# Performance work log

Hardware: AMD Instinct MI355X
Metric: run time of the kernel (lower is better)

The kernel has to match this reference:

```python
import jax, jax.numpy as jnp
import numpy as np

B, S, D, H = 4, 2048, 1024, 16
HD = D // H  # head_dim = 64


def setup_inputs() -> dict:
    key = jax.random.key(0)
    ks = jax.random.split(key, 5)
    scale = 0.02
    return {
        "x": jax.random.normal(ks[0], (B, S, D), dtype=jnp.float32),
        "Wq": jax.random.normal(ks[1], (D, D), dtype=jnp.float32) * scale,
        "Wk": jax.random.normal(ks[2], (D, D), dtype=jnp.float32) * scale,
        "Wv": jax.random.normal(ks[3], (D, D), dtype=jnp.float32) * scale,
        "Wo": jax.random.normal(ks[4], (D, D), dtype=jnp.float32) * scale,
        "bo": jnp.zeros((D,), dtype=jnp.float32),
    }


def reference(x, Wq, Wk, Wv, Wo, bo):
    b, s, d = x.shape
    # projections (no bias on q/k/v, matching qkv_bias=False)
    q = (x @ Wq).reshape(b, s, H, HD).transpose(0, 2, 1, 3)  # [B,H,S,HD]
    k = (x @ Wk).reshape(b, s, H, HD).transpose(0, 2, 1, 3)
    v = (x @ Wv).reshape(b, s, H, HD).transpose(0, 2, 1, 3)
    scores = jnp.einsum("bhqd,bhkd->bhqk", q, k) / jnp.sqrt(jnp.float32(HD))
    causal = jnp.tril(jnp.ones((s, s), dtype=bool))  # True = keep
    scores = jnp.where(causal, scores, -jnp.inf)
    attn = jax.nn.softmax(scores, axis=-1)
    # dropout p=0.0 -> identity
    out = jnp.einsum("bhqk,bhkd->bhqd", attn, v)
    out = out.transpose(0, 2, 1, 3).reshape(b, s, d)
    return out @ Wo + bo
```

## Files before the change

kernel.cpp:

```cpp
#include <hip/hip_runtime.h>

typedef unsigned short u16;
typedef unsigned int u32;
typedef __attribute__((ext_vector_type(4))) float f32x4;
typedef __attribute__((ext_vector_type(8))) __bf16 bf16x8;
typedef __attribute__((ext_vector_type(4))) _Float16 f16x4;
typedef __attribute__((ext_vector_type(4))) u16 u16x4;
typedef __attribute__((ext_vector_type(4))) u32 u32x4;
typedef __attribute__((ext_vector_type(2))) u32 u32x2;

#define D_ 1024
#define S_ 2048
#define B_ 4
#define H_ 16
#define HD_ 64
#define M_ 8192
#define LDP 72
#define QSCALE 0.18033688011112042591f

__device__ __forceinline__ u16 f2bf(float f) {
  u32 u = __float_as_uint(f);
  u += 0x7fffu + ((u >> 16) & 1u);
  return (u16)(u >> 16);
}

__device__ __forceinline__ float max3f(float a, float b, float c) {
  return fmaxf(fmaxf(a, b), c);
}

__device__ __forceinline__ void gload_lds16(const void* g, void* l) {
  __builtin_amdgcn_global_load_lds((const __attribute__((address_space(1))) void*)g,
                                   (__attribute__((address_space(3))) void*)l, 16, 0, 0);
}

__global__ __launch_bounds__(256) void cast_x_kernel(const float* __restrict__ x,
                                                     u16* __restrict__ xb) {
  int i = (blockIdx.x * 256 + threadIdx.x) * 4;
  f32x4 v = *(const f32x4*)(x + i);
  u16x4 o = {f2bf(v[0]), f2bf(v[1]), f2bf(v[2]), f2bf(v[3])};
  *(u16x4*)(xb + i) = o;
}

__global__ __launch_bounds__(256) void wtrans_kernel(const float* __restrict__ Wq, const float* __restrict__ Wk,
                                                     const float* __restrict__ Wv, const float* __restrict__ Wo,
                                                     u16* __restrict__ Wqt, u16* __restrict__ Wkt,
                                                     u16* __restrict__ Wvt, u16* __restrict__ Wot) {
  __shared__ float lds[64][65];
  const float* W = blockIdx.z == 0 ? Wq : blockIdx.z == 1 ? Wk : blockIdx.z == 2 ? Wv : Wo;
  u16* Wt       = blockIdx.z == 0 ? Wqt : blockIdx.z == 1 ? Wkt : blockIdx.z == 2 ? Wvt : Wot;
  int k0 = blockIdx.x * 64, n0 = blockIdx.y * 64;
  int tr = threadIdx.x >> 6, tc = threadIdx.x & 63;
#pragma unroll
  for (int i = 0; i < 16; ++i)
    lds[tr + i * 4][tc] = W[(size_t)(k0 + tr + i * 4) * D_ + n0 + tc];
  __syncthreads();
#pragma unroll
  for (int i = 0; i < 16; ++i)
    Wt[(size_t)(n0 + tr + i * 4) * D_ + k0 + tc] = f2bf(lds[tc][tr + i * 4]);
}

__device__ __forceinline__ void gemm_main(const u16* __restrict__ A, const u16* __restrict__ Bt,
                                          u16* As, u16* Bs, int row0, int col0, f32x4 acc[4][4]) {
  const int tid = threadIdx.x;
  const int lane = tid & 63, wave = tid >> 6;
  const int wr = wave >> 1, wc = wave & 1;
  const int l15 = lane & 15, lg = lane >> 4;
  const int sr8 = lane >> 3;
  const int scx = (lane & 7) ^ sr8;
#pragma unroll 1
  for (int k0 = 0; k0 < D_; k0 += 64) {
#pragma unroll
    for (int it = 0; it < 4; ++it) {
      int rbase = (it * 4 + wave) * 8;
      int r = rbase + sr8;
      gload_lds16(A + (size_t)(row0 + r) * D_ + k0 + scx * 8, As + rbase * 64);
      gload_lds16(Bt + (size_t)(col0 + r) * D_ + k0 + scx * 8, Bs + rbase * 64);
    }
    __syncthreads();
#pragma unroll
    for (int kk = 0; kk < 64; kk += 32) {
      const int cb = kk >> 3;
      bf16x8 af[4], bf[4];
#pragma unroll
      for (int m = 0; m < 4; ++m) {
        int row = wr * 64 + m * 16 + l15;
        af[m] = *(const bf16x8*)(As + row * 64 + (((cb + lg) ^ (l15 & 7)) << 3));
      }
#pragma unroll
      for (int n = 0; n < 4; ++n) {
        int row = wc * 64 + n * 16 + l15;
        bf[n] = *(const bf16x8*)(Bs + row * 64 + (((cb + lg) ^ (l15 & 7)) << 3));
      }
#pragma unroll
      for (int m = 0; m < 4; ++m)
#pragma unroll
        for (int n = 0; n < 4; ++n)
          acc[m][n] = __builtin_amdgcn_mfma_f32_16x16x32_bf16(af[m], bf[n], acc[m][n], 0, 0, 0);
    }
    __syncthreads();
  }
}

__global__ __launch_bounds__(256) void qkv_gemm_kernel(const u16* __restrict__ xb,
                                                       const u16* __restrict__ Wqt, const u16* __restrict__ Wkt,
                                                       const u16* __restrict__ Wvt,
                                                       u16* __restrict__ Qb, u16* __restrict__ Kb,
                                                       _Float16* __restrict__ Vt) {
  __shared__ u16 As[128 * 64];
  __shared__ u16 Bs[128 * 64];
  int lin = blockIdx.x;
  int xcd = lin & 7, pos = lin >> 3;
  int mode = pos / 64;
  int rem = pos & 63;
  int by = xcd * 8 + (rem >> 3);
  int bx = rem & 7;
  const u16* Bt = mode == 0 ? Wqt : mode == 1 ? Wkt : Wvt;
  f32x4 acc[4][4] = {};
  int row0 = by * 128, col0 = bx * 128;
  gemm_main(xb, Bt, As, Bs, row0, col0, acc);
  int lane = threadIdx.x & 63, wave = threadIdx.x >> 6;
  int wr = wave >> 1, wc = wave & 1, l15 = lane & 15, lg = lane >> 4;
  int rbase = row0 + wr * 64 + lg * 4, cbase = col0 + wc * 64 + l15;
  if (mode == 2) {
#pragma unroll
    for (int m = 0; m < 4; ++m) {
      int row = rbase + m * 16;
      int b = row >> 11, s = row & (S_ - 1);
#pragma unroll
      for (int n = 0; n < 4; ++n) {
        int col = cbase + n * 16;
        int h = col >> 6, hd = col & 63;
        f16x4 vv = {(_Float16)acc[m][n][0], (_Float16)acc[m][n][1],
                    (_Float16)acc[m][n][2], (_Float16)acc[m][n][3]};
        *(f16x4*)(Vt + ((size_t)((b << 4) + h) * HD_ + hd) * S_ + s) = vv;
      }
    }
  } else {
    u16* dst = mode == 0 ? Qb : Kb;
    float scl = mode == 0 ? QSCALE : 1.0f;
#pragma unroll
    for (int m = 0; m < 4; ++m)
#pragma unroll
      for (int n = 0; n < 4; ++n) {
        int col = cbase + n * 16;
#pragma unroll
        for (int r = 0; r < 4; ++r) {
          int row = rbase + m * 16 + r;
          dst[(size_t)row * D_ + col] = f2bf(acc[m][n][r] * scl);
        }
      }
  }
}

__global__ __launch_bounds__(256) void attn_kernel(const u16* __restrict__ Qb, const u16* __restrict__ Kb,
                                                   const _Float16* __restrict__ Vt, u16* __restrict__ attnb) {
  __shared__ u16 Ks[2][64][LDP];
  __shared__ _Float16 Vs[2][HD_][LDP];
  const int tid = threadIdx.x;
  const int wave = tid >> 6, lane = tid & 63;
  const int l15 = lane & 15, lg = lane >> 4;
  const int lin = blockIdx.x;
  const int xcd = lin & 7, slot = lin >> 3;
  const int p = slot >> 3;
  const int bh = (slot & 7) * 8 + xcd;
  const int b = bh >> 4, h = bh & 15;

  const int srow = tid >> 3;
  const int scol = (tid & 7) * 8;
  const u16* Kg = Kb + (size_t)(b * S_) * D_ + h * HD_;
  const _Float16* Vg = Vt + (size_t)bh * HD_ * S_;

  const f16x4 ones16 = {(_Float16)1.0f, (_Float16)1.0f, (_Float16)1.0f, (_Float16)1.0f};

#pragma unroll 1
  for (int phase = 0; phase < 2; ++phase) {
    const int qblk = phase == 0 ? (31 - p) : p;
    const int q0b = qblk * 64;
    const int ntiles = qblk + 1;
    const int q0 = q0b + wave * 16;

    const u16* Qrow = Qb + (size_t)(b * S_ + q0 + l15) * D_ + h * HD_;
    bf16x8 qf0 = *(const bf16x8*)(Qrow + lg * 8);
    bf16x8 qf1 = *(const bf16x8*)(Qrow + 32 + lg * 8);

    float m = -1e30f;
    f32x4 o[4] = {};
    f32x4 osum = {};
    u32x4 kreg0, kreg1, vreg0, vreg1;

    __syncthreads();
    kreg0 = *(const u32x4*)(Kg + (size_t)(srow) * D_ + scol);
    kreg1 = *(const u32x4*)(Kg + (size_t)(32 + srow) * D_ + scol);
    vreg0 = *(const u32x4*)(Vg + (size_t)srow * S_ + scol);
    vreg1 = *(const u32x4*)(Vg + (size_t)(32 + srow) * S_ + scol);
    *(u32x4*)(&Ks[0][srow][scol]) = kreg0;
    *(u32x4*)(&Ks[0][32 + srow][scol]) = kreg1;
    *(u32x4*)(&Vs[0][srow][scol]) = vreg0;
    *(u32x4*)(&Vs[0][32 + srow][scol]) = vreg1;

#pragma unroll 1
    for (int t = 0; t < ntiles; ++t) {
      const int cur = t & 1;
      __syncthreads();
      if (t + 1 < ntiles) {
        int kv0n = (t + 1) * 64;
        kreg0 = *(const u32x4*)(Kg + (size_t)(kv0n + srow) * D_ + scol);
        kreg1 = *(const u32x4*)(Kg + (size_t)(kv0n + 32 + srow) * D_ + scol);
        vreg0 = *(const u32x4*)(Vg + (size_t)srow * S_ + kv0n + scol);
        vreg1 = *(const u32x4*)(Vg + (size_t)(32 + srow) * S_ + kv0n + scol);
      }
      f32x4 s[4];
      __builtin_amdgcn_s_setprio(1);
#pragma unroll
      for (int j = 0; j < 4; ++j) {
        bf16x8 kf0 = *(const bf16x8*)(&Ks[cur][j * 16 + l15][lg * 8]);
        bf16x8 kf1 = *(const bf16x8*)(&Ks[cur][j * 16 + l15][32 + lg * 8]);
        f32x4 z = {0.f, 0.f, 0.f, 0.f};
        z = __builtin_amdgcn_mfma_f32_16x16x32_bf16(kf0, qf0, z, 0, 0, 0);
        z = __builtin_amdgcn_mfma_f32_16x16x32_bf16(kf1, qf1, z, 0, 0, 0);
        s[j] = z;
      }
      __builtin_amdgcn_s_setprio(0);
      if (t == ntiles - 1) {
        int qr = wave * 16 + l15;
#pragma unroll
        for (int j = 0; j < 4; ++j)
#pragma unroll
          for (int r = 0; r < 4; ++r)
            if (j * 16 + lg * 4 + r > qr) s[j][r] = -1e30f;
      }
      float x0 = max3f(s[0][0], s[0][1], s[0][2]);
      float x1 = max3f(s[0][3], s[1][0], s[1][1]);
      float x2 = max3f(s[1][2], s[1][3], s[2][0]);
      float x3 = max3f(s[2][1], s[2][2], s[2][3]);
      float x4 = max3f(s[3][0], s[3][1], s[3][2]);
      float tmax = fmaxf(max3f(x0, x1, x2), max3f(x3, x4, s[3][3]));
      tmax = fmaxf(tmax, __shfl_xor(tmax, 16));
      tmax = fmaxf(tmax, __shfl_xor(tmax, 32));
      if (!__all(tmax - m <= 8.f)) {
        float nm = fmaxf(m, tmax);
        float alpha = exp2f(m - nm);
        m = nm;
        osum *= alpha;
#pragma unroll
        for (int hf = 0; hf < 4; ++hf) o[hf] *= alpha;
      }
      f16x4 pb[4];
#pragma unroll
      for (int j = 0; j < 4; ++j) {
        float p0 = exp2f(s[j][0] - m), p1 = exp2f(s[j][1] - m);
        float p2 = exp2f(s[j][2] - m), p3 = exp2f(s[j][3] - m);
        u32 lo = __builtin_bit_cast(u32, __builtin_amdgcn_cvt_pkrtz(p0, p1));
        u32 hi = __builtin_bit_cast(u32, __builtin_amdgcn_cvt_pkrtz(p2, p3));
        pb[j] = __builtin_bit_cast(f16x4, (u32x2){lo, hi});
      }
      __builtin_amdgcn_s_setprio(1);
#pragma unroll
      for (int j = 0; j < 4; ++j) {
#pragma unroll
        for (int hf = 0; hf < 4; ++hf) {
          f16x4 vf = *(const f16x4*)(&Vs[cur][hf * 16 + l15][j * 16 + lg * 4]);
          o[hf] = __builtin_amdgcn_mfma_f32_16x16x16f16(vf, pb[j], o[hf], 0, 0, 0);
        }
        osum = __builtin_amdgcn_mfma_f32_16x16x16f16(ones16, pb[j], osum, 0, 0, 0);
      }
      __builtin_amdgcn_s_setprio(0);
      if (t + 1 < ntiles) {
        const int nxt = cur ^ 1;
        *(u32x4*)(&Ks[nxt][srow][scol]) = kreg0;
        *(u32x4*)(&Ks[nxt][32 + srow][scol]) = kreg1;
        *(u32x4*)(&Vs[nxt][srow][scol]) = vreg0;
        *(u32x4*)(&Vs[nxt][32 + srow][scol]) = vreg1;
      }
    }
    float inv = 1.0f / osum[0];
    u16* Orow = attnb + (size_t)(b * S_ + q0 + l15) * D_ + h * HD_ + lg * 4;
#pragma unroll
    for (int hf = 0; hf < 4; ++hf) {
      u16x4 ov = {f2bf(o[hf][0] * inv), f2bf(o[hf][1] * inv),
                  f2bf(o[hf][2] * inv), f2bf(o[hf][3] * inv)};
      *(u16x4*)(Orow + hf * 16) = ov;
    }
  }
}

__global__ __launch_bounds__(256) void out_gemm_kernel(const u16* __restrict__ attnb, const u16* __restrict__ Wot,
                                                       const float* __restrict__ bo, float* __restrict__ outp) {
  __shared__ u16 As[128 * 64];
  __shared__ u16 Bs[128 * 64];
  int lin = blockIdx.x;
  int xcd = lin & 7, pos = lin >> 3;
  int by = xcd * 8 + (pos >> 3);
  int bx = pos & 7;
  f32x4 acc[4][4] = {};
  int row0 = by * 128, col0 = bx * 128;
  gemm_main(attnb, Wot, As, Bs, row0, col0, acc);
  int lane = threadIdx.x & 63, wave = threadIdx.x >> 6;
  int wr = wave >> 1, wc = wave & 1, l15 = lane & 15, lg = lane >> 4;
  int rbase = row0 + wr * 64 + lg * 4, cbase = col0 + wc * 64 + l15;
#pragma unroll
  for (int n = 0; n < 4; ++n) {
    float bn = bo[cbase + n * 16];
#pragma unroll
    for (int m = 0; m < 4; ++m)
#pragma unroll
      for (int r = 0; r < 4; ++r)
        outp[(size_t)(rbase + m * 16 + r) * D_ + cbase + n * 16] = acc[m][n][r] + bn;
  }
}

extern "C" void kernel_launch(void* const* d_in, const int* in_sizes, int n_in,
                              void* d_out, int out_size, void* d_ws, size_t ws_size,
                              hipStream_t stream) {
  const float* x  = (const float*)d_in[0];
  const float* Wq = (const float*)d_in[1];
  const float* Wk = (const float*)d_in[2];
  const float* Wv = (const float*)d_in[3];
  const float* Wo = (const float*)d_in[4];
  const float* bo = (const float*)d_in[5];
  float* outp = (float*)d_out;

  char* ws = (char*)d_ws;
  u16* xb        = (u16*)(ws);
  u16* Wqt       = (u16*)(ws + ((size_t)16 << 20));
  u16* Wkt       = (u16*)(ws + ((size_t)18 << 20));
  u16* Wvt       = (u16*)(ws + ((size_t)20 << 20));
  u16* Wot       = (u16*)(ws + ((size_t)22 << 20));
  u16* Qb        = (u16*)(ws + ((size_t)24 << 20));
  u16* Kb        = (u16*)(ws + ((size_t)40 << 20));
  _Float16* Vt   = (_Float16*)(ws + ((size_t)56 << 20));
  u16* attnb     = (u16*)(ws + ((size_t)72 << 20));

  cast_x_kernel<<<dim3(M_ * D_ / (256 * 4)), dim3(256), 0, stream>>>(x, xb);
  wtrans_kernel<<<dim3(16, 16, 4), dim3(256), 0, stream>>>(Wq, Wk, Wv, Wo, Wqt, Wkt, Wvt, Wot);
  qkv_gemm_kernel<<<dim3(1536), dim3(256), 0, stream>>>(xb, Wqt, Wkt, Wvt, Qb, Kb, Vt);
  attn_kernel<<<dim3(1024), dim3(256), 0, stream>>>(Qb, Kb, Vt, attnb);
  out_gemm_kernel<<<dim3(512), dim3(256), 0, stream>>>(attnb, Wot, bo, outp);
}
```

Measured before the change: 210.9 us.

## Process both causal query blocks in one KV pass with direct-to-LDS swizzled loads

The attention kernel now walks the KV sequence once and computes the two paired query blocks (long and short) together, so early K/V tiles loaded into LDS are reused for both and not reloaded in a second phase. K/V tiles move to LDS through global_load_lds with an XOR-swizzled, unpadded layout in place of staging through registers and padded arrays. This removes a redundant KV stream and register round-trips. In exchange it raises register pressure (two sets of accumulators and Q fragments) and adds per-tile branching on whether the short block is still active.

```diff
diff --git a/kernel.cpp b/kernel.cpp
--- a/kernel.cpp
+++ b/kernel.cpp
@@ -15,7 +15,6 @@
 #define H_ 16
 #define HD_ 64
 #define M_ 8192
-#define LDP 72
 #define QSCALE 0.18033688011112042591f
 
 __device__ __forceinline__ u16 f2bf(float f) {
@@ -154,8 +153,8 @@
 
 __global__ __launch_bounds__(256) void attn_kernel(const u16* __restrict__ Qb, const u16* __restrict__ Kb,
                                                    const _Float16* __restrict__ Vt, u16* __restrict__ attnb) {
-  __shared__ u16 Ks[2][64][LDP];
-  __shared__ _Float16 Vs[2][HD_][LDP];
+  __shared__ u16 Ks[2][64][64];
+  __shared__ _Float16 Vs[2][64][64];
   const int tid = threadIdx.x;
   const int wave = tid >> 6, lane = tid & 63;
   const int l15 = lane & 15, lg = lane >> 4;
@@ -164,71 +163,90 @@
   const int p = slot >> 3;
   const int bh = (slot & 7) * 8 + xcd;
   const int b = bh >> 4, h = bh & 15;
-
-  const int srow = tid >> 3;
-  const int scol = (tid & 7) * 8;
+  const int ntA = 32 - p, ntB = p + 1;
+  const int q0A = (31 - p) * 64 + wave * 16;
+  const int q0B = p * 64 + wave * 16;
+
   const u16* Kg = Kb + (size_t)(b * S_) * D_ + h * HD_;
   const _Float16* Vg = Vt + (size_t)bh * HD_ * S_;
 
+  const int srow = lane >> 3;
+  const int scs = (lane & 7) ^ srow;
+  const int wr0 = wave * 8;
+
+  const u16* QrowA = Qb + (size_t)(b * S_ + q0A + l15) * D_ + h * HD_;
+  bf16x8 qA0 = *(const bf16x8*)(QrowA + lg * 8);
+  bf16x8 qA1 = *(const bf16x8*)(QrowA + 32 + lg * 8);
+  const u16* QrowB = Qb + (size_t)(b * S_ + q0B + l15) * D_ + h * HD_;
+  bf16x8 qB0 = *(const bf16x8*)(QrowB + lg * 8);
+  bf16x8 qB1 = *(const bf16x8*)(QrowB + 32 + lg * 8);
+
+  float mA = -1e30f, mB = -1e30f;
+  f32x4 oA[4] = {}, oB[4] = {};
+  f32x4 osA = {}, osB = {};
   const f16x4 ones16 = {(_Float16)1.0f, (_Float16)1.0f, (_Float16)1.0f, (_Float16)1.0f};
 
+  const int rx = l15 & 7;
+  const int kc0 = (lg ^ rx) << 3;
+  const int kc1 = kc0 ^ 32;
+  const int lgh = lg >> 1, lgb = (lg & 1) * 4;
+  const int qrm = wave * 16 + l15;
+
+  gload_lds16(Kg + (size_t)(wr0 + srow) * D_ + scs * 8, &Ks[0][wr0][0]);
+  gload_lds16(Kg + (size_t)(32 + wr0 + srow) * D_ + scs * 8, &Ks[0][32 + wr0][0]);
+  gload_lds16(Vg + (size_t)(wr0 + srow) * S_ + scs * 8, &Vs[0][wr0][0]);
+  gload_lds16(Vg + (size_t)(32 + wr0 + srow) * S_ + scs * 8, &Vs[0][32 + wr0][0]);
+
 #pragma unroll 1
-  for (int phase = 0; phase < 2; ++phase) {
-    const int qblk = phase == 0 ? (31 - p) : p;
-    const int q0b = qblk * 64;
-    const int ntiles = qblk + 1;
-    const int q0 = q0b + wave * 16;
-
-    const u16* Qrow = Qb + (size_t)(b * S_ + q0 + l15) * D_ + h * HD_;
-    bf16x8 qf0 = *(const bf16x8*)(Qrow + lg * 8);
-    bf16x8 qf1 = *(const bf16x8*)(Qrow + 32 + lg * 8);
-
-    float m = -1e30f;
-    f32x4 o[4] = {};
-    f32x4 osum = {};
-    u32x4 kreg0, kreg1, vreg0, vreg1;
-
+  for (int t = 0; t < ntA; ++t) {
+    const int cur = t & 1;
     __syncthreads();
-    kreg0 = *(const u32x4*)(Kg + (size_t)(srow) * D_ + scol);
-    kreg1 = *(const u32x4*)(Kg + (size_t)(32 + srow) * D_ + scol);
-    vreg0 = *(const u32x4*)(Vg + (size_t)srow * S_ + scol);
-    vreg1 = *(const u32x4*)(Vg + (size_t)(32 + srow) * S_ + scol);
-    *(u32x4*)(&Ks[0][srow][scol]) = kreg0;
-    *(u32x4*)(&Ks[0][32 + srow][scol]) = kreg1;
-    *(u32x4*)(&Vs[0][srow][scol]) = vreg0;
-    *(u32x4*)(&Vs[0][32 + srow][scol]) = vreg1;
-
-#pragma unroll 1
-    for (int t = 0; t < ntiles; ++t) {
-      const int cur = t & 1;
-      __syncthreads();
-      if (t + 1 < ntiles) {
-        int kv0n = (t + 1) * 64;
-        kreg0 = *(const u32x4*)(Kg + (size_t)(kv0n + srow) * D_ + scol);
-        kreg1 = *(const u32x4*)(Kg + (size_t)(kv0n + 32 + srow) * D_ + scol);
-        vreg0 = *(const u32x4*)(Vg + (size_t)srow * S_ + kv0n + scol);
-        vreg1 = *(const u32x4*)(Vg + (size_t)(32 + srow) * S_ + kv0n + scol);
-      }
-      f32x4 s[4];
-      __builtin_amdgcn_s_setprio(1);
-#pragma unroll
-      for (int j = 0; j < 4; ++j) {
-        bf16x8 kf0 = *(const bf16x8*)(&Ks[cur][j * 16 + l15][lg * 8]);
-        bf16x8 kf1 = *(const bf16x8*)(&Ks[cur][j * 16 + l15][32 + lg * 8]);
-        f32x4 z = {0.f, 0.f, 0.f, 0.f};
-        z = __builtin_amdgcn_mfma_f32_16x16x32_bf16(kf0, qf0, z, 0, 0, 0);
-        z = __builtin_amdgcn_mfma_f32_16x16x32_bf16(kf1, qf1, z, 0, 0, 0);
-        s[j] = z;
-      }
-      __builtin_amdgcn_s_setprio(0);
-      if (t == ntiles - 1) {
-        int qr = wave * 16 + l15;
-#pragma unroll
-        for (int j = 0; j < 4; ++j)
-#pragma unroll
-          for (int r = 0; r < 4; ++r)
-            if (j * 16 + lg * 4 + r > qr) s[j][r] = -1e30f;
-      }
+    if (t + 1 < ntA) {
+      const int kv0 = (t + 1) * 64;
+      const int nxt = cur ^ 1;
+      gload_lds16(Kg + (size_t)(kv0 + wr0 + srow) * D_ + scs * 8, &Ks[nxt][wr0][0]);
+      gload_lds16(Kg + (size_t)(kv0 + 32 + wr0 + srow) * D_ + scs * 8, &Ks[nxt][32 + wr0][0]);
+      gload_lds16(Vg + (size_t)(wr0 + srow) * S_ + kv0 + scs * 8, &Vs[nxt][wr0][0]);
+      gload_lds16(Vg + (size_t)(32 + wr0 + srow) * S_ + kv0 + scs * 8, &Vs[nxt][32 + wr0][0]);
+    }
+    const bool actB = t < ntB;
+
+    f32x4 sA[4], sB[4];
+    __builtin_amdgcn_s_setprio(1);
+#pragma unroll
+    for (int j = 0; j < 4; ++j) {
+      const u16* krow = &Ks[cur][j * 16 + l15][0];
+      bf16x8 kf0 = *(const bf16x8*)(krow + kc0);
+      bf16x8 kf1 = *(const bf16x8*)(krow + kc1);
+      f32x4 zA = {0.f, 0.f, 0.f, 0.f};
+      zA = __builtin_amdgcn_mfma_f32_16x16x32_bf16(kf0, qA0, zA, 0, 0, 0);
+      zA = __builtin_amdgcn_mfma_f32_16x16x32_bf16(kf1, qA1, zA, 0, 0, 0);
+      sA[j] = zA;
+      if (actB) {
+        f32x4 zB = {0.f, 0.f, 0.f, 0.f};
+        zB = __builtin_amdgcn_mfma_f32_16x16x32_bf16(kf0, qB0, zB, 0, 0, 0);
+        zB = __builtin_amdgcn_mfma_f32_16x16x32_bf16(kf1, qB1, zB, 0, 0, 0);
+        sB[j] = zB;
+      }
+    }
+    __builtin_amdgcn_s_setprio(0);
+
+    if (t == ntA - 1) {
+#pragma unroll
+      for (int j = 0; j < 4; ++j)
+#pragma unroll
+        for (int r = 0; r < 4; ++r)
+          if (j * 16 + lg * 4 + r > qrm) sA[j][r] = -1e30f;
+    }
+    if (actB && t == ntB - 1) {
+#pragma unroll
+      for (int j = 0; j < 4; ++j)
+#pragma unroll
+        for (int r = 0; r < 4; ++r)
+          if (j * 16 + lg * 4 + r > qrm) sB[j][r] = -1e30f;
+    }
+
+    auto softmax = [&](f32x4 s[4], float& mm, f32x4 oo[4], f32x4& osum, f16x4 pb[4]) {
       float x0 = max3f(s[0][0], s[0][1], s[0][2]);
       float x1 = max3f(s[0][3], s[1][0], s[1][1]);
       float x2 = max3f(s[1][2], s[1][3], s[2][0]);
@@ -237,48 +255,61 @@
       float tmax = fmaxf(max3f(x0, x1, x2), max3f(x3, x4, s[3][3]));
       tmax = fmaxf(tmax, __shfl_xor(tmax, 16));
       tmax = fmaxf(tmax, __shfl_xor(tmax, 32));
-      if (!__all(tmax - m <= 8.f)) {
-        float nm = fmaxf(m, tmax);
-        float alpha = exp2f(m - nm);
-        m = nm;
+      if (!__all(tmax - mm <= 8.f)) {
+        float nm = fmaxf(mm, tmax);
+        float alpha = exp2f(mm - nm);
+        mm = nm;
         osum *= alpha;
 #pragma unroll
-        for (int hf = 0; hf < 4; ++hf) o[hf] *= alpha;
-      }
-      f16x4 pb[4];
+        for (int hf = 0; hf < 4; ++hf) oo[hf] *= alpha;
+      }
 #pragma unroll
       for (int j = 0; j < 4; ++j) {
-        float p0 = exp2f(s[j][0] - m), p1 = exp2f(s[j][1] - m);
-        float p2 = exp2f(s[j][2] - m), p3 = exp2f(s[j][3] - m);
+        float p0 = exp2f(s[j][0] - mm), p1 = exp2f(s[j][1] - mm);
+        float p2 = exp2f(s[j][2] - mm), p3 = exp2f(s[j][3] - mm);
         u32 lo = __builtin_bit_cast(u32, __builtin_amdgcn_cvt_pkrtz(p0, p1));
         u32 hi = __builtin_bit_cast(u32, __builtin_amdgcn_cvt_pkrtz(p2, p3));
         pb[j] = __builtin_bit_cast(f16x4, (u32x2){lo, hi});
       }
-      __builtin_amdgcn_s_setprio(1);
-#pragma unroll
-      for (int j = 0; j < 4; ++j) {
-#pragma unroll
-        for (int hf = 0; hf < 4; ++hf) {
-          f16x4 vf = *(const f16x4*)(&Vs[cur][hf * 16 + l15][j * 16 + lg * 4]);
-          o[hf] = __builtin_amdgcn_mfma_f32_16x16x16f16(vf, pb[j], o[hf], 0, 0, 0);
-        }
-        osum = __builtin_amdgcn_mfma_f32_16x16x16f16(ones16, pb[j], osum, 0, 0, 0);
-      }
-      __builtin_amdgcn_s_setprio(0);
-      if (t + 1 < ntiles) {
-        const int nxt = cur ^ 1;
-        *(u32x4*)(&Ks[nxt][srow][scol]) = kreg0;
-        *(u32x4*)(&Ks[nxt][32 + srow][scol]) = kreg1;
-        *(u32x4*)(&Vs[nxt][srow][scol]) = vreg0;
-        *(u32x4*)(&Vs[nxt][32 + srow][scol]) = vreg1;
-      }
-    }
-    float inv = 1.0f / osum[0];
-    u16* Orow = attnb + (size_t)(b * S_ + q0 + l15) * D_ + h * HD_ + lg * 4;
+    };
+
+    f16x4 pbA[4], pbB[4];
+    softmax(sA, mA, oA, osA, pbA);
+    if (actB) softmax(sB, mB, oB, osB, pbB);
+
+    __builtin_amdgcn_s_setprio(1);
+#pragma unroll
+    for (int j = 0; j < 4; ++j) {
+      const int pc = (((2 * j + lgh) ^ rx) << 3) + lgb;
+#pragma unroll
+      for (int hf = 0; hf < 4; ++hf) {
+        f16x4 vf = *(const f16x4*)(&Vs[cur][hf * 16 + l15][0] + pc);
+        oA[hf] = __builtin_amdgcn_mfma_f32_16x16x16f16(vf, pbA[j], oA[hf], 0, 0, 0);
+        if (actB) oB[hf] = __builtin_amdgcn_mfma_f32_16x16x16f16(vf, pbB[j], oB[hf], 0, 0, 0);
+      }
+      osA = __builtin_amdgcn_mfma_f32_16x16x16f16(ones16, pbA[j], osA, 0, 0, 0);
+      if (actB) osB = __builtin_amdgcn_mfma_f32_16x16x16f16(ones16, pbB[j], osB, 0, 0, 0);
+    }
+    __builtin_amdgcn_s_setprio(0);
+  }
+
+  {
+    float inv = 1.0f / osA[0];
+    u16* Orow = attnb + (size_t)(b * S_ + q0A + l15) * D_ + h * HD_ + lg * 4;
 #pragma unroll
     for (int hf = 0; hf < 4; ++hf) {
-      u16x4 ov = {f2bf(o[hf][0] * inv), f2bf(o[hf][1] * inv),
-                  f2bf(o[hf][2] * inv), f2bf(o[hf][3] * inv)};
+      u16x4 ov = {f2bf(oA[hf][0] * inv), f2bf(oA[hf][1] * inv),
+                  f2bf(oA[hf][2] * inv), f2bf(oA[hf][3] * inv)};
+      *(u16x4*)(Orow + hf * 16) = ov;
+    }
+  }
+  {
+    float inv = 1.0f / osB[0];
+    u16* Orow = attnb + (size_t)(b * S_ + q0B + l15) * D_ + h * HD_ + lg * 4;
+#pragma unroll
+    for (int hf = 0; hf < 4; ++hf) {
+      u16x4 ov = {f2bf(oB[hf][0] * inv), f2bf(oB[hf][1] * inv),
+                  f2bf(oB[hf][2] * inv), f2bf(oB[hf][3] * inv)};
       *(u16x4*)(Orow + hf * 16) = ov;
     }
   }
```

Measured after the change: 233.1 us. 1.11x slower.

## Use 512-thread attention blocks over 128-row query tiles, drop the ones-MFMA row sum

Applied to the files above, without the earlier changes.

The attention kernel now runs 8 waves per block, each block covering a 128-row query tile in a single pass. This replaces the earlier two-phase pairing of a long and a short 64-row tile per block, so each block shares one K/V staging stream across 8 waves and halves the per-thread global load count. The softmax denominator is now a scalar sum of the probabilities plus cross-lane shuffles instead of an extra MFMA against a ones vector. The costs are that waves stop being balanced against each other (waves on the first half of the tile skip the final KV tile but still wait at the barriers), and the new launch bounds (512, 8) may limit registers.

```diff
diff --git a/kernel.cpp b/kernel.cpp
--- a/kernel.cpp
+++ b/kernel.cpp
@@ -152,63 +152,50 @@
   }
 }
 
-__global__ __launch_bounds__(256) void attn_kernel(const u16* __restrict__ Qb, const u16* __restrict__ Kb,
-                                                   const _Float16* __restrict__ Vt, u16* __restrict__ attnb) {
+__global__ __launch_bounds__(512, 8) void attn_kernel(const u16* __restrict__ Qb, const u16* __restrict__ Kb,
+                                                      const _Float16* __restrict__ Vt, u16* __restrict__ attnb) {
   __shared__ u16 Ks[2][64][LDP];
-  __shared__ _Float16 Vs[2][HD_][LDP];
+  __shared__ _Float16 Vs[2][64][LDP];
   const int tid = threadIdx.x;
   const int wave = tid >> 6, lane = tid & 63;
   const int l15 = lane & 15, lg = lane >> 4;
   const int lin = blockIdx.x;
   const int xcd = lin & 7, slot = lin >> 3;
-  const int p = slot >> 3;
+  const int qsb = 15 - (slot >> 3);
   const int bh = (slot & 7) * 8 + xcd;
   const int b = bh >> 4, h = bh & 15;
+  const int ntiles = 2 * qsb + 2;
+  const int q0 = qsb * 128 + wave * 16;
+  const int tdiag = q0 >> 6;
 
   const int srow = tid >> 3;
   const int scol = (tid & 7) * 8;
   const u16* Kg = Kb + (size_t)(b * S_) * D_ + h * HD_;
   const _Float16* Vg = Vt + (size_t)bh * HD_ * S_;
 
-  const f16x4 ones16 = {(_Float16)1.0f, (_Float16)1.0f, (_Float16)1.0f, (_Float16)1.0f};
+  const u16* Qrow = Qb + (size_t)(b * S_ + q0 + l15) * D_ + h * HD_;
+  bf16x8 qf0 = *(const bf16x8*)(Qrow + lg * 8);
+  bf16x8 qf1 = *(const bf16x8*)(Qrow + 32 + lg * 8);
+
+  float m = -1e30f, lsum = 0.f;
+  f32x4 o[4] = {};
+  u32x4 kreg, vreg;
+
+  kreg = *(const u32x4*)(Kg + (size_t)srow * D_ + scol);
+  vreg = *(const u32x4*)(Vg + (size_t)srow * S_ + scol);
+  *(u32x4*)(&Ks[0][srow][scol]) = kreg;
+  *(u32x4*)(&Vs[0][srow][scol]) = vreg;
 
 #pragma unroll 1
-  for (int phase = 0; phase < 2; ++phase) {
-    const int qblk = phase == 0 ? (31 - p) : p;
-    const int q0b = qblk * 64;
-    const int ntiles = qblk + 1;
-    const int q0 = q0b + wave * 16;
-
-    const u16* Qrow = Qb + (size_t)(b * S_ + q0 + l15) * D_ + h * HD_;
-    bf16x8 qf0 = *(const bf16x8*)(Qrow + lg * 8);
-    bf16x8 qf1 = *(const bf16x8*)(Qrow + 32 + lg * 8);
-
-    float m = -1e30f;
-    f32x4 o[4] = {};
-    f32x4 osum = {};
-    u32x4 kreg0, kreg1, vreg0, vreg1;
-
+  for (int t = 0; t < ntiles; ++t) {
+    const int cur = t & 1;
     __syncthreads();
-    kreg0 = *(const u32x4*)(Kg + (size_t)(srow) * D_ + scol);
-    kreg1 = *(const u32x4*)(Kg + (size_t)(32 + srow) * D_ + scol);
-    vreg0 = *(const u32x4*)(Vg + (size_t)srow * S_ + scol);
-    vreg1 = *(const u32x4*)(Vg + (size_t)(32 + srow) * S_ + scol);
-    *(u32x4*)(&Ks[0][srow][scol]) = kreg0;
-    *(u32x4*)(&Ks[0][32 + srow][scol]) = kreg1;
-    *(u32x4*)(&Vs[0][srow][scol]) = vreg0;
-    *(u32x4*)(&Vs[0][32 + srow][scol]) = vreg1;
-
-#pragma unroll 1
-    for (int t = 0; t < ntiles; ++t) {
-      const int cur = t & 1;
-      __syncthreads();
-      if (t + 1 < ntiles) {
-        int kv0n = (t + 1) * 64;
-        kreg0 = *(const u32x4*)(Kg + (size_t)(kv0n + srow) * D_ + scol);
-        kreg1 = *(const u32x4*)(Kg + (size_t)(kv0n + 32 + srow) * D_ + scol);
-        vreg0 = *(const u32x4*)(Vg + (size_t)srow * S_ + kv0n + scol);
-        vreg1 = *(const u32x4*)(Vg + (size_t)(32 + srow) * S_ + kv0n + scol);
-      }
+    if (t + 1 < ntiles) {
+      int kv0n = (t + 1) * 64;
+      kreg = *(const u32x4*)(Kg + (size_t)(kv0n + srow) * D_ + scol);
+      vreg = *(const u32x4*)(Vg + (size_t)srow * S_ + kv0n + scol);
+    }
+    if (t <= tdiag) {
       f32x4 s[4];
       __builtin_amdgcn_s_setprio(1);
 #pragma unroll
@@ -221,8 +208,8 @@
         s[j] = z;
       }
       __builtin_amdgcn_s_setprio(0);
-      if (t == ntiles - 1) {
-        int qr = wave * 16 + l15;
+      if (t == tdiag) {
+        int qr = (q0 & 63) + l15;
 #pragma unroll
         for (int j = 0; j < 4; ++j)
 #pragma unroll
@@ -241,7 +228,7 @@
         float nm = fmaxf(m, tmax);
         float alpha = exp2f(m - nm);
         m = nm;
-        osum *= alpha;
+        lsum *= alpha;
 #pragma unroll
         for (int hf = 0; hf < 4; ++hf) o[hf] *= alpha;
       }
@@ -250,6 +237,7 @@
       for (int j = 0; j < 4; ++j) {
         float p0 = exp2f(s[j][0] - m), p1 = exp2f(s[j][1] - m);
         float p2 = exp2f(s[j][2] - m), p3 = exp2f(s[j][3] - m);
+        lsum += (p0 + p1) + (p2 + p3);
         u32 lo = __builtin_bit_cast(u32, __builtin_amdgcn_cvt_pkrtz(p0, p1));
         u32 hi = __builtin_bit_cast(u32, __builtin_amdgcn_cvt_pkrtz(p2, p3));
         pb[j] = __builtin_bit_cast(f16x4, (u32x2){lo, hi});
@@ -262,25 +250,24 @@
           f16x4 vf = *(const f16x4*)(&Vs[cur][hf * 16 + l15][j * 16 + lg * 4]);
           o[hf] = __builtin_amdgcn_mfma_f32_16x16x16f16(vf, pb[j], o[hf], 0, 0, 0);
         }
-        osum = __builtin_amdgcn_mfma_f32_16x16x16f16(ones16, pb[j], osum, 0, 0, 0);
       }
       __builtin_amdgcn_s_setprio(0);
-      if (t + 1 < ntiles) {
-        const int nxt = cur ^ 1;
-        *(u32x4*)(&Ks[nxt][srow][scol]) = kreg0;
-        *(u32x4*)(&Ks[nxt][32 + srow][scol]) = kreg1;
-        *(u32x4*)(&Vs[nxt][srow][scol]) = vreg0;
-        *(u32x4*)(&Vs[nxt][32 + srow][scol]) = vreg1;
-      }
-    }
-    float inv = 1.0f / osum[0];
-    u16* Orow = attnb + (size_t)(b * S_ + q0 + l15) * D_ + h * HD_ + lg * 4;
-#pragma unroll
-    for (int hf = 0; hf < 4; ++hf) {
-      u16x4 ov = {f2bf(o[hf][0] * inv), f2bf(o[hf][1] * inv),
-                  f2bf(o[hf][2] * inv), f2bf(o[hf][3] * inv)};
-      *(u16x4*)(Orow + hf * 16) = ov;
-    }
+    }
+    if (t + 1 < ntiles) {
+      const int nxt = cur ^ 1;
+      *(u32x4*)(&Ks[nxt][srow][scol]) = kreg;
+      *(u32x4*)(&Vs[nxt][srow][scol]) = vreg;
+    }
+  }
+  lsum += __shfl_xor(lsum, 16);
+  lsum += __shfl_xor(lsum, 32);
+  float inv = 1.0f / lsum;
+  u16* Orow = attnb + (size_t)(b * S_ + q0 + l15) * D_ + h * HD_ + lg * 4;
+#pragma unroll
+  for (int hf = 0; hf < 4; ++hf) {
+    u16x4 ov = {f2bf(o[hf][0] * inv), f2bf(o[hf][1] * inv),
+                f2bf(o[hf][2] * inv), f2bf(o[hf][3] * inv)};
+    *(u16x4*)(Orow + hf * 16) = ov;
   }
 }
 
@@ -334,6 +321,6 @@
   cast_x_kernel<<<dim3(M_ * D_ / (256 * 4)), dim3(256), 0, stream>>>(x, xb);
   wtrans_kernel<<<dim3(16, 16, 4), dim3(256), 0, stream>>>(Wq, Wk, Wv, Wo, Wqt, Wkt, Wvt, Wot);
   qkv_gemm_kernel<<<dim3(1536), dim3(256), 0, stream>>>(xb, Wqt, Wkt, Wvt, Qb, Kb, Vt);
-  attn_kernel<<<dim3(1024), dim3(256), 0, stream>>>(Qb, Kb, Vt, attnb);
+  attn_kernel<<<dim3(1024), dim3(512), 0, stream>>>(Qb, Kb, Vt, attnb);
   out_gemm_kernel<<<dim3(512), dim3(256), 0, stream>>>(attnb, Wot, bo, outp);
 }
```

Result: slower. 244.1 us (+15.8%).

## Split paired-phase attention blocks into one q-block per workgroup with single-buffered LDS

Applied to the files above, without the earlier changes.

Each attention workgroup now handles a single 64-row query block instead of a balanced long/short pair, and the grid doubles to 2048, ordered longest-first. LDS drops from double to single buffered (prefetch into registers, store, sync), and the row-sum MFMA with a ones vector becomes a scalar accumulation plus a shuffle reduction. Launch bounds request 8 waves per EU for higher occupancy. The costs are an extra barrier per tile, less overlap of LDS writes with compute, and reliance on the hardware scheduler to balance the uneven causal work.

```diff
diff --git a/kernel.cpp b/kernel.cpp
--- a/kernel.cpp
+++ b/kernel.cpp
@@ -152,135 +152,120 @@
   }
 }
 
-__global__ __launch_bounds__(256) void attn_kernel(const u16* __restrict__ Qb, const u16* __restrict__ Kb,
-                                                   const _Float16* __restrict__ Vt, u16* __restrict__ attnb) {
-  __shared__ u16 Ks[2][64][LDP];
-  __shared__ _Float16 Vs[2][HD_][LDP];
+__global__ __launch_bounds__(256, 8) void attn_kernel(const u16* __restrict__ Qb, const u16* __restrict__ Kb,
+                                                      const _Float16* __restrict__ Vt, u16* __restrict__ attnb) {
+  __shared__ u16 Ks[64][LDP];
+  __shared__ _Float16 Vs[64][LDP];
   const int tid = threadIdx.x;
   const int wave = tid >> 6, lane = tid & 63;
   const int l15 = lane & 15, lg = lane >> 4;
   const int lin = blockIdx.x;
   const int xcd = lin & 7, slot = lin >> 3;
-  const int p = slot >> 3;
+  const int qblk = 31 - (slot >> 3);
   const int bh = (slot & 7) * 8 + xcd;
   const int b = bh >> 4, h = bh & 15;
+  const int ntiles = qblk + 1;
+  const int q0 = qblk * 64 + wave * 16;
 
   const int srow = tid >> 3;
   const int scol = (tid & 7) * 8;
   const u16* Kg = Kb + (size_t)(b * S_) * D_ + h * HD_;
   const _Float16* Vg = Vt + (size_t)bh * HD_ * S_;
 
-  const f16x4 ones16 = {(_Float16)1.0f, (_Float16)1.0f, (_Float16)1.0f, (_Float16)1.0f};
+  const u16* Qrow = Qb + (size_t)(b * S_ + q0 + l15) * D_ + h * HD_;
+  bf16x8 qf0 = *(const bf16x8*)(Qrow + lg * 8);
+  bf16x8 qf1 = *(const bf16x8*)(Qrow + 32 + lg * 8);
+
+  float m = -1e30f, lsum = 0.f;
+  f32x4 o[4] = {};
+  u32x4 kreg0, kreg1, vreg0, vreg1;
+
+  kreg0 = *(const u32x4*)(Kg + (size_t)(srow) * D_ + scol);
+  kreg1 = *(const u32x4*)(Kg + (size_t)(32 + srow) * D_ + scol);
+  vreg0 = *(const u32x4*)(Vg + (size_t)srow * S_ + scol);
+  vreg1 = *(const u32x4*)(Vg + (size_t)(32 + srow) * S_ + scol);
 
 #pragma unroll 1
-  for (int phase = 0; phase < 2; ++phase) {
-    const int qblk = phase == 0 ? (31 - p) : p;
-    const int q0b = qblk * 64;
-    const int ntiles = qblk + 1;
-    const int q0 = q0b + wave * 16;
-
-    const u16* Qrow = Qb + (size_t)(b * S_ + q0 + l15) * D_ + h * HD_;
-    bf16x8 qf0 = *(const bf16x8*)(Qrow + lg * 8);
-    bf16x8 qf1 = *(const bf16x8*)(Qrow + 32 + lg * 8);
-
-    float m = -1e30f;
-    f32x4 o[4] = {};
-    f32x4 osum = {};
-    u32x4 kreg0, kreg1, vreg0, vreg1;
-
+  for (int t = 0; t < ntiles; ++t) {
     __syncthreads();
-    kreg0 = *(const u32x4*)(Kg + (size_t)(srow) * D_ + scol);
-    kreg1 = *(const u32x4*)(Kg + (size_t)(32 + srow) * D_ + scol);
-    vreg0 = *(const u32x4*)(Vg + (size_t)srow * S_ + scol);
-    vreg1 = *(const u32x4*)(Vg + (size_t)(32 + srow) * S_ + scol);
-    *(u32x4*)(&Ks[0][srow][scol]) = kreg0;
-    *(u32x4*)(&Ks[0][32 + srow][scol]) = kreg1;
-    *(u32x4*)(&Vs[0][srow][scol]) = vreg0;
-    *(u32x4*)(&Vs[0][32 + srow][scol]) = vreg1;
-
-#pragma unroll 1
-    for (int t = 0; t < ntiles; ++t) {
-      const int cur = t & 1;
-      __syncthreads();
-      if (t + 1 < ntiles) {
-        int kv0n = (t + 1) * 64;
-        kreg0 = *(const u32x4*)(Kg + (size_t)(kv0n + srow) * D_ + scol);
-        kreg1 = *(const u32x4*)(Kg + (size_t)(kv0n + 32 + srow) * D_ + scol);
-        vreg0 = *(const u32x4*)(Vg + (size_t)srow * S_ + kv0n + scol);
-        vreg1 = *(const u32x4*)(Vg + (size_t)(32 + srow) * S_ + kv0n + scol);
-      }
-      f32x4 s[4];
-      __builtin_amdgcn_s_setprio(1);
-#pragma unroll
-      for (int j = 0; j < 4; ++j) {
-        bf16x8 kf0 = *(const bf16x8*)(&Ks[cur][j * 16 + l15][lg * 8]);
-        bf16x8 kf1 = *(const bf16x8*)(&Ks[cur][j * 16 + l15][32 + lg * 8]);
-        f32x4 z = {0.f, 0.f, 0.f, 0.f};
-        z = __builtin_amdgcn_mfma_f32_16x16x32_bf16(kf0, qf0, z, 0, 0, 0);
-        z = __builtin_amdgcn_mfma_f32_16x16x32_bf16(kf1, qf1, z, 0, 0, 0);
-        s[j] = z;
-      }
-      __builtin_amdgcn_s_setprio(0);
-      if (t == ntiles - 1) {
-        int qr = wave * 16 + l15;
-#pragma unroll
-        for (int j = 0; j < 4; ++j)
-#pragma unroll
-          for (int r = 0; r < 4; ++r)
-            if (j * 16 + lg * 4 + r > qr) s[j][r] = -1e30f;
-      }
-      float x0 = max3f(s[0][0], s[0][1], s[0][2]);
-      float x1 = max3f(s[0][3], s[1][0], s[1][1]);
-      float x2 = max3f(s[1][2], s[1][3], s[2][0]);
-      float x3 = max3f(s[2][1], s[2][2], s[2][3]);
-      float x4 = max3f(s[3][0], s[3][1], s[3][2]);
-      float tmax = fmaxf(max3f(x0, x1, x2), max3f(x3, x4, s[3][3]));
-      tmax = fmaxf(tmax, __shfl_xor(tmax, 16));
-      tmax = fmaxf(tmax, __shfl_xor(tmax, 32));
-      if (!__all(tmax - m <= 8.f)) {
-        float nm = fmaxf(m, tmax);
-        float alpha = exp2f(m - nm);
-        m = nm;
-        osum *= alpha;
-#pragma unroll
-        for (int hf = 0; hf < 4; ++hf) o[hf] *= alpha;
-      }
-      f16x4 pb[4];
-#pragma unroll
-      for (int j = 0; j < 4; ++j) {
-        float p0 = exp2f(s[j][0] - m), p1 = exp2f(s[j][1] - m);
-        float p2 = exp2f(s[j][2] - m), p3 = exp2f(s[j][3] - m);
-        u32 lo = __builtin_bit_cast(u32, __builtin_amdgcn_cvt_pkrtz(p0, p1));
-        u32 hi = __builtin_bit_cast(u32, __builtin_amdgcn_cvt_pkrtz(p2, p3));
-        pb[j] = __builtin_bit_cast(f16x4, (u32x2){lo, hi});
-      }
-      __builtin_amdgcn_s_setprio(1);
-#pragma unroll
-      for (int j = 0; j < 4; ++j) {
-#pragma unroll
-        for (int hf = 0; hf < 4; ++hf) {
-          f16x4 vf = *(const f16x4*)(&Vs[cur][hf * 16 + l15][j * 16 + lg * 4]);
-          o[hf] = __builtin_amdgcn_mfma_f32_16x16x16f16(vf, pb[j], o[hf], 0, 0, 0);
-        }
-        osum = __builtin_amdgcn_mfma_f32_16x16x16f16(ones16, pb[j], osum, 0, 0, 0);
-      }
-      __builtin_amdgcn_s_setprio(0);
-      if (t + 1 < ntiles) {
-        const int nxt = cur ^ 1;
-        *(u32x4*)(&Ks[nxt][srow][scol]) = kreg0;
-        *(u32x4*)(&Ks[nxt][32 + srow][scol]) = kreg1;
-        *(u32x4*)(&Vs[nxt][srow][scol]) = vreg0;
-        *(u32x4*)(&Vs[nxt][32 + srow][scol]) = vreg1;
-      }
-    }
-    float inv = 1.0f / osum[0];
-    u16* Orow = attnb + (size_t)(b * S_ + q0 + l15) * D_ + h * HD_ + lg * 4;
-#pragma unroll
-    for (int hf = 0; hf < 4; ++hf) {
-      u16x4 ov = {f2bf(o[hf][0] * inv), f2bf(o[hf][1] * inv),
-                  f2bf(o[hf][2] * inv), f2bf(o[hf][3] * inv)};
-      *(u16x4*)(Orow + hf * 16) = ov;
-    }
+    *(u32x4*)(&Ks[srow][scol]) = kreg0;
+    *(u32x4*)(&Ks[32 + srow][scol]) = kreg1;
+    *(u32x4*)(&Vs[srow][scol]) = vreg0;
+    *(u32x4*)(&Vs[32 + srow][scol]) = vreg1;
+    __syncthreads();
+    if (t + 1 < ntiles) {
+      int kv0n = (t + 1) * 64;
+      kreg0 = *(const u32x4*)(Kg + (size_t)(kv0n + srow) * D_ + scol);
+      kreg1 = *(const u32x4*)(Kg + (size_t)(kv0n + 32 + srow) * D_ + scol);
+      vreg0 = *(const u32x4*)(Vg + (size_t)srow * S_ + kv0n + scol);
+      vreg1 = *(const u32x4*)(Vg + (size_t)(32 + srow) * S_ + kv0n + scol);
+    }
+    f32x4 s[4];
+    __builtin_amdgcn_s_setprio(1);
+#pragma unroll
+    for (int j = 0; j < 4; ++j) {
+      bf16x8 kf0 = *(const bf16x8*)(&Ks[j * 16 + l15][lg * 8]);
+      bf16x8 kf1 = *(const bf16x8*)(&Ks[j * 16 + l15][32 + lg * 8]);
+      f32x4 z = {0.f, 0.f, 0.f, 0.f};
+      z = __builtin_amdgcn_mfma_f32_16x16x32_bf16(kf0, qf0, z, 0, 0, 0);
+      z = __builtin_amdgcn_mfma_f32_16x16x32_bf16(kf1, qf1, z, 0, 0, 0);
+      s[j] = z;
+    }
+    __builtin_amdgcn_s_setprio(0);
+    if (t == ntiles - 1) {
+      int qr = wave * 16 + l15;
+#pragma unroll
+      for (int j = 0; j < 4; ++j)
+#pragma unroll
+        for (int r = 0; r < 4; ++r)
+          if (j * 16 + lg * 4 + r > qr) s[j][r] = -1e30f;
+    }
+    float x0 = max3f(s[0][0], s[0][1], s[0][2]);
+    float x1 = max3f(s[0][3], s[1][0], s[1][1]);
+    float x2 = max3f(s[1][2], s[1][3], s[2][0]);
+    float x3 = max3f(s[2][1], s[2][2], s[2][3]);
+    float x4 = max3f(s[3][0], s[3][1], s[3][2]);
+    float tmax = fmaxf(max3f(x0, x1, x2), max3f(x3, x4, s[3][3]));
+    tmax = fmaxf(tmax, __shfl_xor(tmax, 16));
+    tmax = fmaxf(tmax, __shfl_xor(tmax, 32));
+    if (!__all(tmax - m <= 8.f)) {
+      float nm = fmaxf(m, tmax);
+      float alpha = exp2f(m - nm);
+      m = nm;
+      lsum *= alpha;
+#pragma unroll
+      for (int hf = 0; hf < 4; ++hf) o[hf] *= alpha;
+    }
+    f16x4 pb[4];
+#pragma unroll
+    for (int j = 0; j < 4; ++j) {
+      float p0 = exp2f(s[j][0] - m), p1 = exp2f(s[j][1] - m);
+      float p2 = exp2f(s[j][2] - m), p3 = exp2f(s[j][3] - m);
+      lsum += (p0 + p1) + (p2 + p3);
+      u32 lo = __builtin_bit_cast(u32, __builtin_amdgcn_cvt_pkrtz(p0, p1));
+      u32 hi = __builtin_bit_cast(u32, __builtin_amdgcn_cvt_pkrtz(p2, p3));
+      pb[j] = __builtin_bit_cast(f16x4, (u32x2){lo, hi});
+    }
+    __builtin_amdgcn_s_setprio(1);
+#pragma unroll
+    for (int j = 0; j < 4; ++j) {
+#pragma unroll
+      for (int hf = 0; hf < 4; ++hf) {
+        f16x4 vf = *(const f16x4*)(&Vs[hf * 16 + l15][j * 16 + lg * 4]);
+        o[hf] = __builtin_amdgcn_mfma_f32_16x16x16f16(vf, pb[j], o[hf], 0, 0, 0);
+      }
+    }
+    __builtin_amdgcn_s_setprio(0);
+  }
+  lsum += __shfl_xor(lsum, 16);
+  lsum += __shfl_xor(lsum, 32);
+  float inv = 1.0f / lsum;
+  u16* Orow = attnb + (size_t)(b * S_ + q0 + l15) * D_ + h * HD_ + lg * 4;
+#pragma unroll
+  for (int hf = 0; hf < 4; ++hf) {
+    u16x4 ov = {f2bf(o[hf][0] * inv), f2bf(o[hf][1] * inv),
+                f2bf(o[hf][2] * inv), f2bf(o[hf][3] * inv)};
+    *(u16x4*)(Orow + hf * 16) = ov;
   }
 }
 
@@ -334,6 +319,6 @@
   cast_x_kernel<<<dim3(M_ * D_ / (256 * 4)), dim3(256), 0, stream>>>(x, xb);
   wtrans_kernel<<<dim3(16, 16, 4), dim3(256), 0, stream>>>(Wq, Wk, Wv, Wo, Wqt, Wkt, Wvt, Wot);
   qkv_gemm_kernel<<<dim3(1536), dim3(256), 0, stream>>>(xb, Wqt, Wkt, Wvt, Qb, Kb, Vt);
-  attn_kernel<<<dim3(1024), dim3(256), 0, stream>>>(Qb, Kb, Vt, attnb);
+  attn_kernel<<<dim3(2048), dim3(256), 0, stream>>>(Qb, Kb, Vt, attnb);
   out_gemm_kernel<<<dim3(512), dim3(256), 0, stream>>>(attnb, Wot, bo, outp);
 }
```

Result: slower. 354.3 us (+68.0%).
